# Kernel optimization log

Measured on AMD Instinct MI355X. Metric: run time of the kernel, lower is better.

The kernel has to match this reference:

```python
import jax, jax.numpy as jnp
import numpy as np

H = 64  # LSTM hidden size (hardcoded in Baseline)

def _lstm_encode(x, W_ih, W_hh, b_ih, b_hh):
    # x: [N, C, T] -> final hidden state [N, H]
    # PyTorch LSTMCell gate order: i, f, g, o
    N = x.shape[0]
    xs = jnp.moveaxis(x, 2, 0)                       # [T, N, C]
    xp = jnp.einsum('tnc,gc->tng', xs, W_ih) + b_ih  # precompute input proj [T, N, 4H]
    h0 = jnp.zeros((N, H), dtype=x.dtype)
    c0 = jnp.zeros((N, H), dtype=x.dtype)

    def step(carry, xp_t):
        h, c = carry
        g = xp_t + h @ W_hh.T + b_hh                 # [N, 4H]
        i, f, gg, o = jnp.split(g, 4, axis=-1)
        c = jax.nn.sigmoid(f) * c + jax.nn.sigmoid(i) * jnp.tanh(gg)
        h = jax.nn.sigmoid(o) * jnp.tanh(c)
        return (h, c), None

    (h, _), _ = jax.lax.scan(step, (h0, c0), xp)
    return h

def _head(x, W1, b1, W2, b2, W3, b3):
    # dropout is identity at inference; relu on first two layers, none on last
    x = jax.nn.relu(x @ W1.T + b1)
    x = jax.nn.relu(x @ W2.T + b2)
    return x @ W3.T + b3

def setup_inputs() -> dict:
    key = jax.random.key(0)
    ks = jax.random.split(key, 24)
    C1, C2 = 32, 56
    N, T = 8192, 72
    d = {
        'X_obs': jax.random.normal(ks[0], (N, C1, T), jnp.float32),
        'X_wrf_cmaq': jax.random.normal(ks[1], (N, C2, T), jnp.float32),
        'obs_Wih': jax.random.normal(ks[2], (4 * H, C1), jnp.float32) * 0.1,
        'obs_Whh': jax.random.normal(ks[3], (4 * H, H), jnp.float32) * 0.1,
        'obs_bih': jax.random.normal(ks[4], (4 * H,), jnp.float32) * 0.1,
        'obs_bhh': jax.random.normal(ks[5], (4 * H,), jnp.float32) * 0.1,
        'wrf_Wih': jax.random.normal(ks[6], (4 * H, C2), jnp.float32) * 0.1,
        'wrf_Whh': jax.random.normal(ks[7], (4 * H, H), jnp.float32) * 0.1,
        'wrf_bih': jax.random.normal(ks[8], (4 * H,), jnp.float32) * 0.1,
        'wrf_bhh': jax.random.normal(ks[9], (4 * H,), jnp.float32) * 0.1,
    }
    dims = [(96, 128), (64, 96), (48, 64)]
    k = 10
    for head in ('fsp', 'o3'):
        for li, (o, i) in enumerate(dims, 1):
            d[f'{head}_W{li}'] = jax.random.normal(ks[k], (o, i), jnp.float32) * (1.0 / np.sqrt(i)); k += 1
            d[f'{head}_b{li}'] = jax.random.normal(ks[k], (o,), jnp.float32) * 0.05; k += 1
    return d

def reference(X_obs, X_wrf_cmaq,
              obs_Wih, obs_Whh, obs_bih, obs_bhh,
              wrf_Wih, wrf_Whh, wrf_bih, wrf_bhh,
              fsp_W1, fsp_b1, fsp_W2, fsp_b2, fsp_W3, fsp_b3,
              o3_W1, o3_b1, o3_W2, o3_b2, o3_W3, o3_b3):
    h_obs = _lstm_encode(X_obs, obs_Wih, obs_Whh, obs_bih, obs_bhh)
    h_wrf = _lstm_encode(X_wrf_cmaq, wrf_Wih, wrf_Whh, wrf_bih, wrf_bhh)
    feat = jnp.concatenate([h_obs, h_wrf], axis=1)  # [N, 128]
    fsp = _head(feat, fsp_W1, fsp_b1, fsp_W2, fsp_b2, fsp_W3, fsp_b3)
    o3 = _head(feat, o3_W1, o3_b1, o3_W2, o3_b2, o3_W3, o3_b3)
    return jnp.stack([fsp, o3], axis=1)  # [N, 2, 48]
```

## Files before the change

### kernel.cpp

```cpp
#include <hip/hip_runtime.h>

typedef __attribute__((ext_vector_type(8))) short short8;
typedef __attribute__((ext_vector_type(4))) float f32x4;

#define OFF_BXO   64
#define OFF_BHO   (OFF_BXO + 16384)
#define OFF_BXW   (OFF_BHO + 32768)
#define OFF_BHW   (OFF_BXW + 32768)
#define OFF_HW    (OFF_BHW + 32768)
#define OFF_BIASL (OFF_HW + 43008)
#define OFF_BIASH (OFF_BIASL + 1024)
#define OFF_FEAT  (OFF_BIASH + 832)

__device__ __forceinline__ float b2f(unsigned short u) {
    return __uint_as_float(((unsigned)u) << 16);
}
__device__ __forceinline__ unsigned short f2b(float f) {
    unsigned u = __float_as_uint(f);
    u += 0x7FFFu + ((u >> 16) & 1u);
    return (unsigned short)(u >> 16);
}
__device__ __forceinline__ float ldin(const void* p, int idx, int isf) {
    return isf ? ((const float*)p)[idx] : b2f(((const unsigned short*)p)[idx]);
}
__device__ __forceinline__ float sigmoidf_(float x) {
    return __builtin_amdgcn_rcpf(1.0f + __expf(-x));
}
__device__ __forceinline__ float tanhf_(float x) {
    return 2.0f * __builtin_amdgcn_rcpf(1.0f + __expf(-2.0f * x)) - 1.0f;
}
__device__ __forceinline__ f32x4 MFMA(short8 a, short8 b, f32x4 c) {
    return __builtin_amdgcn_mfma_f32_16x16x32_bf16(a, b, c, 0, 0, 0);
}

__global__ __launch_bounds__(256) void detect_kernel(
    const unsigned short* __restrict__ X, int* __restrict__ flag)
{
    __shared__ int cnt[256];
    int c = 0;
    for (int i = threadIdx.x; i < 2048; i += 256) {
        unsigned short u = X[2 * i];
        c += (((u >> 7) & 0xFF) >= 192);
    }
    cnt[threadIdx.x] = c;
    __syncthreads();
    if (threadIdx.x == 0) {
        int s = 0;
        for (int i = 0; i < 256; ++i) s += cnt[i];
        *flag = (s > 64) ? 1 : 0;
    }
}

__global__ __launch_bounds__(256) void prep_kernel(
    const void* oWih, const void* oWhh, const void* obih, const void* obhh,
    const void* wWih, const void* wWhh, const void* wbih, const void* wbhh,
    const void* fW1, const void* fb1, const void* fW2, const void* fb2,
    const void* fW3, const void* fb3,
    const void* oW1, const void* ob1, const void* oW2, const void* ob2,
    const void* oW3, const void* ob3,
    unsigned short* __restrict__ ws)
{
    const int isf = ((const int*)ws)[0];
    const int gid = blockIdx.x * 256 + threadIdx.x;
    const int gsz = gridDim.x * 256;

    unsigned short* BXO = ws + OFF_BXO;
    unsigned short* BHO = ws + OFF_BHO;
    unsigned short* BXW = ws + OFF_BXW;
    unsigned short* BHW = ws + OFF_BHW;
    unsigned short* HW  = ws + OFF_HW;

    for (int i = gid; i < 8192; i += gsz) {
        int j = i & 7, lane = (i >> 3) & 63, nt = (i >> 9) & 3, wave = i >> 11;
        int g = nt * 64 + wave * 16 + (lane & 15);
        int k = ((lane >> 4) << 3) + j;
        float w = ldin(oWih, g * 32 + k, isf);
        unsigned short hi = f2b(w);
        BXO[i] = hi; BXO[8192 + i] = f2b(w - b2f(hi));
    }
    for (int i = gid; i < 16384; i += gsz) {
        int j = i & 7, lane = (i >> 3) & 63, nt = (i >> 9) & 3;
        int kt = (i >> 11) & 1, wave = i >> 12;
        int g = nt * 64 + wave * 16 + (lane & 15);
        int k = kt * 32 + ((lane >> 4) << 3) + j;
        float w = ldin(oWhh, g * 64 + k, isf);
        unsigned short hi = f2b(w);
        BHO[i] = hi; BHO[16384 + i] = f2b(w - b2f(hi));
    }
    for (int i = gid; i < 16384; i += gsz) {
        int j = i & 7, lane = (i >> 3) & 63, nt = (i >> 9) & 3;
        int wave = (i >> 11) & 3, kt2 = i >> 13;
        int g = nt * 64 + wave * 16 + (lane & 15);
        int k = kt2 * 32 + ((lane >> 4) << 3) + j;
        float w = (k < 56) ? ldin(wWih, g * 56 + k, isf) : 0.f;
        unsigned short hi = f2b(w);
        BXW[i] = hi; BXW[16384 + i] = f2b(w - b2f(hi));
    }
    for (int i = gid; i < 16384; i += gsz) {
        int j = i & 7, lane = (i >> 3) & 63, nt = (i >> 9) & 3;
        int kt = (i >> 11) & 1, wave = i >> 12;
        int g = nt * 64 + wave * 16 + (lane & 15);
        int k = kt * 32 + ((lane >> 4) << 3) + j;
        float w = ldin(wWhh, g * 64 + k, isf);
        unsigned short hi = f2b(w);
        BHW[i] = hi; BHW[16384 + i] = f2b(w - b2f(hi));
    }
    for (int i = gid; i < 12288; i += gsz) HW[i]         = f2b(ldin(fW1, i, isf));
    for (int i = gid; i < 6144;  i += gsz) HW[12288 + i] = f2b(ldin(fW2, i, isf));
    for (int i = gid; i < 3072;  i += gsz) HW[18432 + i] = f2b(ldin(fW3, i, isf));
    for (int i = gid; i < 12288; i += gsz) HW[21504 + i] = f2b(ldin(oW1, i, isf));
    for (int i = gid; i < 6144;  i += gsz) HW[33792 + i] = f2b(ldin(oW2, i, isf));
    for (int i = gid; i < 3072;  i += gsz) HW[39936 + i] = f2b(ldin(oW3, i, isf));
    float* BL = (float*)(ws + OFF_BIASL);
    for (int i = gid; i < 256; i += gsz) BL[i]       = ldin(obih, i, isf) + ldin(obhh, i, isf);
    for (int i = gid; i < 256; i += gsz) BL[256 + i] = ldin(wbih, i, isf) + ldin(wbhh, i, isf);
    float* BB = (float*)(ws + OFF_BIASH);
    for (int i = gid; i < 96; i += gsz) BB[i]       = ldin(fb1, i, isf);
    for (int i = gid; i < 64; i += gsz) BB[96 + i]  = ldin(fb2, i, isf);
    for (int i = gid; i < 48; i += gsz) BB[160 + i] = ldin(fb3, i, isf);
    for (int i = gid; i < 96; i += gsz) BB[208 + i] = ldin(ob1, i, isf);
    for (int i = gid; i < 64; i += gsz) BB[304 + i] = ldin(ob2, i, isf);
    for (int i = gid; i < 48; i += gsz) BB[368 + i] = ldin(ob3, i, isf);
}

#define TCH 4
__global__ __launch_bounds__(256) void lstm_kernel(
    const void* __restrict__ Xo, const void* __restrict__ Xw,
    unsigned short* __restrict__ ws)
{
    __shared__ unsigned short xbuf[2][TCH][8][16][8];
    __shared__ unsigned short hfrag[2][2][2][4][16][8];

    const int tid  = threadIdx.x;
    const int wave = tid >> 6, lane = tid & 63;
    const int quad = lane >> 4, m16 = lane & 15;
    const bool isw = blockIdx.x >= 512;
    const int blk  = isw ? (int)blockIdx.x - 512 : (int)blockIdx.x;
    const int n0   = blk * 16;
    const int isf  = ((const int*)ws)[0];

    const void* x = isw ? Xw : Xo;
    const unsigned short* BX = ws + (isw ? OFF_BXW : OFF_BXO);
    const unsigned short* BH = ws + (isw ? OFF_BHW : OFF_BHO);
    const float* BL = (const float*)(ws + OFF_BIASL) + (isw ? 256 : 0);
    unsigned short* featH = ws + OFF_FEAT;
    unsigned short* featL = featH + 8192 * 128;
    const int C       = isw ? 56 : 32;
    const int Cpad    = isw ? 64 : 32;
    const int cshift  = isw ? 6 : 5;
    const int xloOff  = isw ? 16384 : 8192;
    const int featOff = isw ? 64 : 0;

    short8 BhH[2][4], BhL[2][4];
#pragma unroll
    for (int kt = 0; kt < 2; ++kt)
#pragma unroll
        for (int nt = 0; nt < 4; ++nt) {
            int idx = ((wave * 2 + kt) * 4 + nt) * 512 + lane * 8;
            BhH[kt][nt] = *(const short8*)&BH[idx];
            BhL[kt][nt] = *(const short8*)&BH[16384 + idx];
        }
    short8 BxH0[4], BxL0[4], BxH1[4], BxL1[4];
#pragma unroll
    for (int nt = 0; nt < 4; ++nt) {
        int idx = (wave * 4 + nt) * 512 + lane * 8;
        BxH0[nt] = *(const short8*)&BX[idx];
        BxL0[nt] = *(const short8*)&BX[xloOff + idx];
    }
    if (isw) {
#pragma unroll
        for (int nt = 0; nt < 4; ++nt) {
            int idx = (wave * 4 + nt) * 512 + lane * 8;
            BxH1[nt] = *(const short8*)&BX[8192 + idx];
            BxL1[nt] = *(const short8*)&BX[xloOff + 8192 + idx];
        }
    }

    const int u = wave * 16 + m16;
    const float bias_i = BL[u];
    const float bias_f = BL[u + 64];
    const float bias_g = BL[u + 128];
    const float bias_o = BL[u + 192];
    float c4[4] = {0.f, 0.f, 0.f, 0.f};

    const int ktw = wave >> 1;
    const int qaw = ((wave & 1) << 1) | (m16 >> 3);
    const int jw  = m16 & 7;
    const int chunkbit = (m16 >> 3) << 2;
    const int prr = ((((m16 & 3) << 2) | (m16 >> 2)) ^ ((quad & 1) << 2));

    for (int i = tid; i < 2 * 2 * 2 * 4 * 16 * 8; i += 256)
        ((unsigned short*)hfrag)[i] = 0;

    int par = 0;
    for (int chunk = 0; chunk < 18; ++chunk) {
        const int t0 = chunk * TCH;
        for (int i = tid; i < (16 << cshift); i += 256) {
            int n = i >> cshift, c = i & (Cpad - 1);
            float v[TCH];
            if (c < C) {
                size_t off = ((size_t)(n0 + n) * C + c) * 72 + t0;
                if (isf) {
                    f32x4 u0 = *(const f32x4*)((const float*)x + off);
                    v[0] = u0[0]; v[1] = u0[1]; v[2] = u0[2]; v[3] = u0[3];
                } else {
                    const unsigned short* p = (const unsigned short*)x + off;
#pragma unroll
                    for (int j = 0; j < TCH; ++j) v[j] = b2f(p[j]);
                }
            } else {
#pragma unroll
                for (int j = 0; j < TCH; ++j) v[j] = 0.f;
            }
            int kt = c >> 3;
            int pr = n ^ kt;
#pragma unroll
            for (int tt = 0; tt < TCH; ++tt) {
                unsigned short hi = f2b(v[tt]);
                xbuf[0][tt][kt][pr][c & 7] = hi;
                xbuf[1][tt][kt][pr][c & 7] = f2b(v[tt] - b2f(hi));
            }
        }
        __syncthreads();

        for (int tt = 0; tt < TCH; ++tt) {
            const int t = t0 + tt;
            f32x4 acc[4] = {{0,0,0,0},{0,0,0,0},{0,0,0,0},{0,0,0,0}};
            {
                short8 axh = *(const short8*)&xbuf[0][tt][quad][m16 ^ quad][0];
                short8 axl = *(const short8*)&xbuf[1][tt][quad][m16 ^ quad][0];
#pragma unroll
                for (int nt = 0; nt < 4; ++nt) {
                    acc[nt] = MFMA(axh, BxH0[nt], acc[nt]);
                    acc[nt] = MFMA(axl, BxH0[nt], acc[nt]);
                    acc[nt] = MFMA(axh, BxL0[nt], acc[nt]);
                }
            }
            if (isw) {
                short8 axh = *(const short8*)&xbuf[0][tt][4 + quad][m16 ^ (4 + quad)][0];
                short8 axl = *(const short8*)&xbuf[1][tt][4 + quad][m16 ^ (4 + quad)][0];
#pragma unroll
                for (int nt = 0; nt < 4; ++nt) {
                    acc[nt] = MFMA(axh, BxH1[nt], acc[nt]);
                    acc[nt] = MFMA(axl, BxH1[nt], acc[nt]);
                    acc[nt] = MFMA(axh, BxL1[nt], acc[nt]);
                }
            }
#pragma unroll
            for (int kt = 0; kt < 2; ++kt) {
                short8 ahi = *(const short8*)&hfrag[par][0][kt][quad][prr][0];
                short8 alo = *(const short8*)&hfrag[par][1][kt][quad][prr][0];
#pragma unroll
                for (int nt = 0; nt < 4; ++nt) {
                    acc[nt] = MFMA(ahi, BhH[kt][nt], acc[nt]);
                    acc[nt] = MFMA(alo, BhH[kt][nt], acc[nt]);
                    acc[nt] = MFMA(ahi, BhL[kt][nt], acc[nt]);
                }
            }

#pragma unroll
            for (int r = 0; r < 4; ++r) {
                float iv = sigmoidf_(acc[0][r] + bias_i);
                float fv = sigmoidf_(acc[1][r] + bias_f);
                float gv = tanhf_(acc[2][r] + bias_g);
                float ov = sigmoidf_(acc[3][r] + bias_o);
                float c  = fv * c4[r] + iv * gv;
                c4[r]    = c;
                float h  = ov * tanhf_(c);
                unsigned hu = __float_as_uint(h);
                unsigned short hi = (unsigned short)(hu >> 16);
                float hiv = __uint_as_float(hu & 0xFFFF0000u);
                unsigned short lo = (unsigned short)(__float_as_uint(h - hiv) >> 16);
                int pr = ((r << 2) | quad) ^ chunkbit;
                hfrag[par ^ 1][0][ktw][qaw][pr][jw] = hi;
                hfrag[par ^ 1][1][ktw][qaw][pr][jw] = lo;
                if (t == 71) {
                    int m = quad * 4 + r;
                    featH[(size_t)(n0 + m) * 128 + featOff + u] = hi;
                    featL[(size_t)(n0 + m) * 128 + featOff + u] = lo;
                }
            }
            __syncthreads();
            par ^= 1;
        }
    }
}

__global__ __launch_bounds__(256) void heads_kernel(
    const unsigned short* __restrict__ ws, void* __restrict__ out)
{
    __shared__ unsigned short afrag[4][4][4][16][8];
    const int tid  = threadIdx.x;
    const int wave = tid >> 6, lane = tid & 63;
    const int quad = lane >> 4, m16 = lane & 15;
    const int r0   = blockIdx.x * 64 + wave * 16;
    const int isf  = ((const int*)ws)[0];

    const unsigned short* HW    = ws + OFF_HW;
    const float*          BB    = (const float*)(ws + OFF_BIASH);
    const unsigned short* featH = ws + OFF_FEAT;
    const unsigned short* featL = featH + 8192 * 128;

    short8 fh[4], fl[4];
#pragma unroll
    for (int kt = 0; kt < 4; ++kt) {
        size_t o = (size_t)(r0 + m16) * 128 + kt * 32 + quad * 8;
        fh[kt] = *(const short8*)&featH[o];
        fl[kt] = *(const short8*)&featL[o];
    }

    for (int head = 0; head < 2; ++head) {
        const unsigned short* W1 = HW + (head ? 21504 : 0);
        const unsigned short* W2 = W1 + 12288;
        const unsigned short* W3 = W2 + 6144;
        const float* b1 = BB + head * 208;
        const float* b2 = b1 + 96;
        const float* b3 = b2 + 64;

        f32x4 a1[6] = {{0,0,0,0},{0,0,0,0},{0,0,0,0},{0,0,0,0},{0,0,0,0},{0,0,0,0}};
#pragma unroll
        for (int kt = 0; kt < 4; ++kt)
#pragma unroll
            for (int nt = 0; nt < 6; ++nt) {
                short8 bw = *(const short8*)
                    &W1[(nt * 16 + m16) * 128 + kt * 32 + quad * 8];
                a1[nt] = MFMA(fh[kt], bw, a1[nt]);
                a1[nt] = MFMA(fl[kt], bw, a1[nt]);
            }
#pragma unroll
        for (int nt = 0; nt < 6; ++nt) {
            int u = nt * 16 + m16;
            float bv = b1[u];
#pragma unroll
            for (int r = 0; r < 4; ++r) {
                float v = a1[nt][r] + bv;
                v = v > 0.f ? v : 0.f;
                afrag[wave][u >> 5][(u >> 3) & 3][quad * 4 + r][u & 7] = f2b(v);
            }
        }
        __syncthreads();

        f32x4 a2[4] = {{0,0,0,0},{0,0,0,0},{0,0,0,0},{0,0,0,0}};
#pragma unroll
        for (int kt = 0; kt < 3; ++kt) {
            short8 a = *(const short8*)&afrag[wave][kt][quad][m16][0];
#pragma unroll
            for (int nt = 0; nt < 4; ++nt) {
                short8 bw = *(const short8*)
                    &W2[(nt * 16 + m16) * 96 + kt * 32 + quad * 8];
                a2[nt] = MFMA(a, bw, a2[nt]);
            }
        }
        __syncthreads();
#pragma unroll
        for (int nt = 0; nt < 4; ++nt) {
            int u = nt * 16 + m16;
            float bv = b2[u];
#pragma unroll
            for (int r = 0; r < 4; ++r) {
                float v = a2[nt][r] + bv;
                v = v > 0.f ? v : 0.f;
                afrag[wave][u >> 5][(u >> 3) & 3][quad * 4 + r][u & 7] = f2b(v);
            }
        }
        __syncthreads();

        f32x4 a3[3] = {{0,0,0,0},{0,0,0,0},{0,0,0,0}};
#pragma unroll
        for (int kt = 0; kt < 2; ++kt) {
            short8 a = *(const short8*)&afrag[wave][kt][quad][m16][0];
#pragma unroll
            for (int nt = 0; nt < 3; ++nt) {
                short8 bw = *(const short8*)
                    &W3[(nt * 16 + m16) * 64 + kt * 32 + quad * 8];
                a3[nt] = MFMA(a, bw, a3[nt]);
            }
        }
#pragma unroll
        for (int nt = 0; nt < 3; ++nt) {
            int u = nt * 16 + m16;
            float bv = b3[u];
#pragma unroll
            for (int r = 0; r < 4; ++r) {
                int row = quad * 4 + r;
                size_t idx = (size_t)(r0 + row) * 96 + head * 48 + u;
                float v = a3[nt][r] + bv;
                if (isf) ((float*)out)[idx] = v;
                else     ((unsigned short*)out)[idx] = f2b(v);
            }
        }
        __syncthreads();
    }
}

extern "C" void kernel_launch(void* const* d_in, const int* in_sizes, int n_in,
                              void* d_out, int out_size, void* d_ws, size_t ws_size,
                              hipStream_t stream)
{
    unsigned short* ws = (unsigned short*)d_ws;

    detect_kernel<<<1, 256, 0, stream>>>((const unsigned short*)d_in[0], (int*)d_ws);
    prep_kernel<<<64, 256, 0, stream>>>(
        d_in[2], d_in[3], d_in[4], d_in[5],
        d_in[6], d_in[7], d_in[8], d_in[9],
        d_in[10], d_in[11], d_in[12], d_in[13], d_in[14], d_in[15],
        d_in[16], d_in[17], d_in[18], d_in[19], d_in[20], d_in[21],
        ws);
    lstm_kernel<<<1024, 256, 0, stream>>>(d_in[0], d_in[1], ws);
    heads_kernel<<<128, 256, 0, stream>>>(ws, d_out);
}
```

Before: 510.8 us.

## Prefetch LSTM inputs into registers, fold gate scaling into weights, split heads blocks

```diff
diff --git a/kernel.cpp b/kernel.cpp
--- a/kernel.cpp
+++ b/kernel.cpp
@@ -12,6 +12,9 @@
 #define OFF_BIASH (OFF_BIASL + 1024)
 #define OFF_FEAT  (OFF_BIASH + 832)
 
+#define SC_IFO  -1.4426950408889634f
+#define SC_G    -2.8853900817779268f
+
 __device__ __forceinline__ float b2f(unsigned short u) {
     return __uint_as_float(((unsigned)u) << 16);
 }
@@ -23,11 +26,12 @@
 __device__ __forceinline__ float ldin(const void* p, int idx, int isf) {
     return isf ? ((const float*)p)[idx] : b2f(((const unsigned short*)p)[idx]);
 }
-__device__ __forceinline__ float sigmoidf_(float x) {
-    return __builtin_amdgcn_rcpf(1.0f + __expf(-x));
-}
-__device__ __forceinline__ float tanhf_(float x) {
-    return 2.0f * __builtin_amdgcn_rcpf(1.0f + __expf(-2.0f * x)) - 1.0f;
+__device__ __forceinline__ float exp2_(float x) {
+#if __has_builtin(__builtin_amdgcn_exp2f)
+    return __builtin_amdgcn_exp2f(x);
+#else
+    return exp2f(x);
+#endif
 }
 __device__ __forceinline__ f32x4 MFMA(short8 a, short8 b, f32x4 c) {
     return __builtin_amdgcn_mfma_f32_16x16x32_bf16(a, b, c, 0, 0, 0);
@@ -74,7 +78,8 @@
         int j = i & 7, lane = (i >> 3) & 63, nt = (i >> 9) & 3, wave = i >> 11;
         int g = nt * 64 + wave * 16 + (lane & 15);
         int k = ((lane >> 4) << 3) + j;
-        float w = ldin(oWih, g * 32 + k, isf);
+        float s = ((g >> 6) == 2) ? SC_G : SC_IFO;
+        float w = ldin(oWih, g * 32 + k, isf) * s;
         unsigned short hi = f2b(w);
         BXO[i] = hi; BXO[8192 + i] = f2b(w - b2f(hi));
     }
@@ -83,7 +88,8 @@
         int kt = (i >> 11) & 1, wave = i >> 12;
         int g = nt * 64 + wave * 16 + (lane & 15);
         int k = kt * 32 + ((lane >> 4) << 3) + j;
-        float w = ldin(oWhh, g * 64 + k, isf);
+        float s = ((g >> 6) == 2) ? SC_G : SC_IFO;
+        float w = ldin(oWhh, g * 64 + k, isf) * s;
         unsigned short hi = f2b(w);
         BHO[i] = hi; BHO[16384 + i] = f2b(w - b2f(hi));
     }
@@ -92,7 +98,8 @@
         int wave = (i >> 11) & 3, kt2 = i >> 13;
         int g = nt * 64 + wave * 16 + (lane & 15);
         int k = kt2 * 32 + ((lane >> 4) << 3) + j;
-        float w = (k < 56) ? ldin(wWih, g * 56 + k, isf) : 0.f;
+        float s = ((g >> 6) == 2) ? SC_G : SC_IFO;
+        float w = (k < 56) ? ldin(wWih, g * 56 + k, isf) * s : 0.f;
         unsigned short hi = f2b(w);
         BXW[i] = hi; BXW[16384 + i] = f2b(w - b2f(hi));
     }
@@ -101,7 +108,8 @@
         int kt = (i >> 11) & 1, wave = i >> 12;
         int g = nt * 64 + wave * 16 + (lane & 15);
         int k = kt * 32 + ((lane >> 4) << 3) + j;
-        float w = ldin(wWhh, g * 64 + k, isf);
+        float s = ((g >> 6) == 2) ? SC_G : SC_IFO;
+        float w = ldin(wWhh, g * 64 + k, isf) * s;
         unsigned short hi = f2b(w);
         BHW[i] = hi; BHW[16384 + i] = f2b(w - b2f(hi));
     }
@@ -112,8 +120,14 @@
     for (int i = gid; i < 6144;  i += gsz) HW[33792 + i] = f2b(ldin(oW2, i, isf));
     for (int i = gid; i < 3072;  i += gsz) HW[39936 + i] = f2b(ldin(oW3, i, isf));
     float* BL = (float*)(ws + OFF_BIASL);
-    for (int i = gid; i < 256; i += gsz) BL[i]       = ldin(obih, i, isf) + ldin(obhh, i, isf);
-    for (int i = gid; i < 256; i += gsz) BL[256 + i] = ldin(wbih, i, isf) + ldin(wbhh, i, isf);
+    for (int i = gid; i < 256; i += gsz) {
+        float s = ((i >> 6) == 2) ? SC_G : SC_IFO;
+        BL[i] = (ldin(obih, i, isf) + ldin(obhh, i, isf)) * s;
+    }
+    for (int i = gid; i < 256; i += gsz) {
+        float s = ((i >> 6) == 2) ? SC_G : SC_IFO;
+        BL[256 + i] = (ldin(wbih, i, isf) + ldin(wbhh, i, isf)) * s;
+    }
     float* BB = (float*)(ws + OFF_BIASH);
     for (int i = gid; i < 96; i += gsz) BB[i]       = ldin(fb1, i, isf);
     for (int i = gid; i < 64; i += gsz) BB[96 + i]  = ldin(fb2, i, isf);
@@ -124,7 +138,7 @@
 }
 
 #define TCH 4
-__global__ __launch_bounds__(256) void lstm_kernel(
+__global__ __launch_bounds__(256, 4) void lstm_kernel(
     const void* __restrict__ Xo, const void* __restrict__ Xw,
     unsigned short* __restrict__ ws)
 {
@@ -148,6 +162,7 @@
     const int C       = isw ? 56 : 32;
     const int Cpad    = isw ? 64 : 32;
     const int cshift  = isw ? 6 : 5;
+    const int niter   = isw ? 4 : 2;
     const int xloOff  = isw ? 16384 : 8192;
     const int featOff = isw ? 64 : 0;
 
@@ -192,40 +207,63 @@
     for (int i = tid; i < 2 * 2 * 2 * 4 * 16 * 8; i += 256)
         ((unsigned short*)hfrag)[i] = 0;
 
+    float pv[4][TCH];
+    auto LOADX = [&](int ch) {
+        const int t0x = ch * TCH;
+#pragma unroll
+        for (int it = 0; it < 4; ++it) {
+            if (it < niter) {
+                int i = tid + it * 256;
+                int n = i >> cshift, c = i & (Cpad - 1);
+                if (c < C) {
+                    size_t off = ((size_t)(n0 + n) * C + c) * 72 + t0x;
+                    if (isf) {
+                        f32x4 u0 = *(const f32x4*)((const float*)x + off);
+                        pv[it][0] = u0[0]; pv[it][1] = u0[1];
+                        pv[it][2] = u0[2]; pv[it][3] = u0[3];
+                    } else {
+                        const unsigned short* p = (const unsigned short*)x + off;
+#pragma unroll
+                        for (int j = 0; j < TCH; ++j) pv[it][j] = b2f(p[j]);
+                    }
+                } else {
+#pragma unroll
+                    for (int j = 0; j < TCH; ++j) pv[it][j] = 0.f;
+                }
+            }
+        }
+    };
+
+    LOADX(0);
     int par = 0;
     for (int chunk = 0; chunk < 18; ++chunk) {
-        const int t0 = chunk * TCH;
-        for (int i = tid; i < (16 << cshift); i += 256) {
-            int n = i >> cshift, c = i & (Cpad - 1);
-            float v[TCH];
-            if (c < C) {
-                size_t off = ((size_t)(n0 + n) * C + c) * 72 + t0;
-                if (isf) {
-                    f32x4 u0 = *(const f32x4*)((const float*)x + off);
-                    v[0] = u0[0]; v[1] = u0[1]; v[2] = u0[2]; v[3] = u0[3];
-                } else {
-                    const unsigned short* p = (const unsigned short*)x + off;
-#pragma unroll
-                    for (int j = 0; j < TCH; ++j) v[j] = b2f(p[j]);
-                }
-            } else {
-#pragma unroll
-                for (int j = 0; j < TCH; ++j) v[j] = 0.f;
-            }
-            int kt = c >> 3;
-            int pr = n ^ kt;
-#pragma unroll
-            for (int tt = 0; tt < TCH; ++tt) {
-                unsigned short hi = f2b(v[tt]);
-                xbuf[0][tt][kt][pr][c & 7] = hi;
-                xbuf[1][tt][kt][pr][c & 7] = f2b(v[tt] - b2f(hi));
-            }
-        }
-        __syncthreads();
+#pragma unroll
+        for (int it = 0; it < 4; ++it) {
+            if (it < niter) {
+                int i = tid + it * 256;
+                int n = i >> cshift, c = i & (Cpad - 1);
+                int kt = c >> 3, pr = n ^ kt;
+#pragma unroll
+                for (int tt = 0; tt < TCH; ++tt) {
+                    float v = pv[it][tt];
+                    unsigned hu = __float_as_uint(v);
+                    unsigned short hi = (unsigned short)(hu >> 16);
+                    float hiv = __uint_as_float(hu & 0xFFFF0000u);
+                    unsigned short lo = (unsigned short)(__float_as_uint(v - hiv) >> 16);
+                    xbuf[0][tt][kt][pr][c & 7] = hi;
+                    xbuf[1][tt][kt][pr][c & 7] = lo;
+                }
+            }
+        }
+        asm volatile("s_waitcnt lgkmcnt(0)\ns_barrier" ::: "memory");
+        if (chunk < 17) LOADX(chunk + 1);
 
         for (int tt = 0; tt < TCH; ++tt) {
-            const int t = t0 + tt;
-            f32x4 acc[4] = {{0,0,0,0},{0,0,0,0},{0,0,0,0},{0,0,0,0}};
+            const int t = chunk * TCH + tt;
+            f32x4 acc[4] = {{bias_i, bias_i, bias_i, bias_i},
+                            {bias_f, bias_f, bias_f, bias_f},
+                            {bias_g, bias_g, bias_g, bias_g},
+                            {bias_o, bias_o, bias_o, bias_o}};
             {
                 short8 axh = *(const short8*)&xbuf[0][tt][quad][m16 ^ quad][0];
                 short8 axl = *(const short8*)&xbuf[1][tt][quad][m16 ^ quad][0];
@@ -260,13 +298,14 @@
 
 #pragma unroll
             for (int r = 0; r < 4; ++r) {
-                float iv = sigmoidf_(acc[0][r] + bias_i);
-                float fv = sigmoidf_(acc[1][r] + bias_f);
-                float gv = tanhf_(acc[2][r] + bias_g);
-                float ov = sigmoidf_(acc[3][r] + bias_o);
+                float iv = __builtin_amdgcn_rcpf(1.0f + exp2_(acc[0][r]));
+                float fv = __builtin_amdgcn_rcpf(1.0f + exp2_(acc[1][r]));
+                float gv = 2.0f * __builtin_amdgcn_rcpf(1.0f + exp2_(acc[2][r])) - 1.0f;
+                float ov = __builtin_amdgcn_rcpf(1.0f + exp2_(acc[3][r]));
                 float c  = fv * c4[r] + iv * gv;
                 c4[r]    = c;
-                float h  = ov * tanhf_(c);
+                float tc = 2.0f * __builtin_amdgcn_rcpf(1.0f + exp2_(c * SC_G)) - 1.0f;
+                float h  = ov * tc;
                 unsigned hu = __float_as_uint(h);
                 unsigned short hi = (unsigned short)(hu >> 16);
                 float hiv = __uint_as_float(hu & 0xFFFF0000u);
@@ -280,20 +319,19 @@
                     featL[(size_t)(n0 + m) * 128 + featOff + u] = lo;
                 }
             }
-            __syncthreads();
+            asm volatile("s_waitcnt lgkmcnt(0)\ns_barrier" ::: "memory");
             par ^= 1;
         }
     }
 }
 
-__global__ __launch_bounds__(256) void heads_kernel(
+__global__ __launch_bounds__(64) void heads_kernel(
     const unsigned short* __restrict__ ws, void* __restrict__ out)
 {
-    __shared__ unsigned short afrag[4][4][4][16][8];
-    const int tid  = threadIdx.x;
-    const int wave = tid >> 6, lane = tid & 63;
+    __shared__ unsigned short afrag[4][4][16][8];
+    const int lane = threadIdx.x;
     const int quad = lane >> 4, m16 = lane & 15;
-    const int r0   = blockIdx.x * 64 + wave * 16;
+    const int r0   = blockIdx.x * 16;
     const int isf  = ((const int*)ws)[0];
 
     const unsigned short* HW    = ws + OFF_HW;
@@ -335,15 +373,15 @@
             for (int r = 0; r < 4; ++r) {
                 float v = a1[nt][r] + bv;
                 v = v > 0.f ? v : 0.f;
-                afrag[wave][u >> 5][(u >> 3) & 3][quad * 4 + r][u & 7] = f2b(v);
-            }
-        }
-        __syncthreads();
+                afrag[u >> 5][(u >> 3) & 3][quad * 4 + r][u & 7] = f2b(v);
+            }
+        }
+        asm volatile("s_waitcnt lgkmcnt(0)" ::: "memory");
 
         f32x4 a2[4] = {{0,0,0,0},{0,0,0,0},{0,0,0,0},{0,0,0,0}};
 #pragma unroll
         for (int kt = 0; kt < 3; ++kt) {
-            short8 a = *(const short8*)&afrag[wave][kt][quad][m16][0];
+            short8 a = *(const short8*)&afrag[kt][quad][m16][0];
 #pragma unroll
             for (int nt = 0; nt < 4; ++nt) {
                 short8 bw = *(const short8*)
@@ -351,7 +389,7 @@
                 a2[nt] = MFMA(a, bw, a2[nt]);
             }
         }
-        __syncthreads();
+        asm volatile("s_waitcnt lgkmcnt(0)" ::: "memory");
 #pragma unroll
         for (int nt = 0; nt < 4; ++nt) {
             int u = nt * 16 + m16;
@@ -360,15 +398,15 @@
             for (int r = 0; r < 4; ++r) {
                 float v = a2[nt][r] + bv;
                 v = v > 0.f ? v : 0.f;
-                afrag[wave][u >> 5][(u >> 3) & 3][quad * 4 + r][u & 7] = f2b(v);
-            }
-        }
-        __syncthreads();
+                afrag[u >> 5][(u >> 3) & 3][quad * 4 + r][u & 7] = f2b(v);
+            }
+        }
+        asm volatile("s_waitcnt lgkmcnt(0)" ::: "memory");
 
         f32x4 a3[3] = {{0,0,0,0},{0,0,0,0},{0,0,0,0}};
 #pragma unroll
         for (int kt = 0; kt < 2; ++kt) {
-            short8 a = *(const short8*)&afrag[wave][kt][quad][m16][0];
+            short8 a = *(const short8*)&afrag[kt][quad][m16][0];
 #pragma unroll
             for (int nt = 0; nt < 3; ++nt) {
                 short8 bw = *(const short8*)
@@ -389,7 +427,7 @@
                 else     ((unsigned short*)out)[idx] = f2b(v);
             }
         }
-        __syncthreads();
+        asm volatile("s_waitcnt lgkmcnt(0)" ::: "memory");
     }
 }
 
@@ -407,5 +445,5 @@
         d_in[16], d_in[17], d_in[18], d_in[19], d_in[20], d_in[21],
         ws);
     lstm_kernel<<<1024, 256, 0, stream>>>(d_in[0], d_in[1], ws);
-    heads_kernel<<<128, 256, 0, stream>>>(ws, d_out);
-}
+    heads_kernel<<<512, 64, 0, stream>>>(ws, d_out);
+}
```

Result: slower. 1.315 ms (+157.4%).
